# Optimization experiments

Hardware: AMD Instinct MI355X
Metric: run time of the kernel (lower is better)

The kernel has to match this reference:

```python
import jax, jax.numpy as jnp
import numpy as np

B, S, D, H, FF = 4, 2048, 1024, 16, 4096
DT, TARGET, ITERS = 0.1, 0.0, 5


def _ln(x, w, b):
    mu = jnp.mean(x, axis=-1, keepdims=True)
    var = jnp.mean((x - mu) ** 2, axis=-1, keepdims=True)
    return (x - mu) * jax.lax.rsqrt(var + 1e-5) * w + b


def setup_inputs() -> dict:
    key = jax.random.key(0)
    ks = iter(jax.random.split(key, 16))
    w = lambda shape: jax.random.normal(next(ks), shape, dtype=jnp.float32) * 0.02
    return {
        "x": jax.random.normal(next(ks), (B, S, D), dtype=jnp.float32),
        "ln_attn_w": jnp.ones((D,), jnp.float32), "ln_attn_b": jnp.zeros((D,), jnp.float32),
        "attn_in_w": w((3 * D, D)), "attn_in_b": jnp.zeros((3 * D,), jnp.float32),
        "attn_out_w": w((D, D)), "attn_out_b": jnp.zeros((D,), jnp.float32),
        "ln1_w": jnp.ones((D,), jnp.float32), "ln1_b": jnp.zeros((D,), jnp.float32),
        "ln2_w": jnp.ones((D,), jnp.float32), "ln2_b": jnp.zeros((D,), jnp.float32),
        "inl_u_w": w((D, D)), "inl_u_b": jnp.zeros((D,), jnp.float32),
        "inl_a_w": w((D, D)), "inl_a_b": jnp.zeros((D,), jnp.float32),
        "inl_b_w": w((D, D)), "inl_b_b": jnp.zeros((D,), jnp.float32),
        "inl_g_w": w((D, D)), "inl_g_b": jnp.zeros((D,), jnp.float32),
        "ff1_w": w((FF, D)), "ff1_b": jnp.zeros((FF,), jnp.float32),
        "ff2_w": w((D, FF)), "ff2_b": jnp.zeros((D,), jnp.float32),
    }


def reference(x, ln_attn_w, ln_attn_b, attn_in_w, attn_in_b, attn_out_w, attn_out_b,
              ln1_w, ln1_b, ln2_w, ln2_b,
              inl_u_w, inl_u_b, inl_a_w, inl_a_b, inl_b_w, inl_b_b, inl_g_w, inl_g_b,
              ff1_w, ff1_b, ff2_w, ff2_b):
    dh = D // H
    scale = 1.0 / np.sqrt(dh).astype(np.float32)
    # --- causal multi-head attention (dropout = identity, eval mode) ---
    xn = _ln(x, ln_attn_w, ln_attn_b)
    qkv = xn @ attn_in_w.T + attn_in_b            # [B,S,3D]
    q, k, v = jnp.split(qkv, 3, axis=-1)
    hsplit = lambda t: t.reshape(B, S, H, dh).transpose(0, 2, 1, 3)  # [B,H,S,dh]
    q, k, v = hsplit(q), hsplit(k), hsplit(v)
    scores = jnp.einsum('bhqd,bhkd->bhqk', q, k) * scale
    causal = jnp.triu(jnp.ones((S, S), dtype=bool), 1)
    scores = jnp.where(causal, jnp.finfo(scores.dtype).min, scores)
    probs = jax.nn.softmax(scores, axis=-1)
    attn_out = jnp.einsum('bhqk,bhkd->bhqd', probs, v).transpose(0, 2, 1, 3).reshape(B, S, D)
    attn_out = attn_out @ attn_out_w.T + attn_out_b
    x = x + attn_out
    context = attn_out
    # --- INL integrator dynamics (controllers depend only on context) ---
    xs = _ln(x, ln1_w, ln1_b)
    vs = jnp.zeros_like(xs)
    u = context @ inl_u_w.T + inl_u_b
    alpha = jax.nn.sigmoid(context @ inl_a_w.T + inl_a_b)
    beta = jax.nn.softplus(context @ inl_b_w.T + inl_b_b)
    g = jax.nn.sigmoid(context @ inl_g_w.T + inl_g_b)
    for _ in range(ITERS):
        vs = vs + DT * (alpha * (TARGET - xs) - beta * vs + u)
        xs = xs + DT * g * vs
    x = x + xs
    # --- feed-forward (exact GELU as torch default) ---
    h = _ln(x, ln2_w, ln2_b)
    x = x + (jax.nn.gelu(h @ ff1_w.T + ff1_b, approximate=False) @ ff2_w.T + ff2_b)
    return x
```

## Files before the change

kernel.cpp:

```cpp
#include <hip/hip_runtime.h>
#include <cstdint>
#include <cmath>

typedef __attribute__((ext_vector_type(4))) float floatx4;
typedef __attribute__((ext_vector_type(8))) __bf16 bf16x8;
typedef __attribute__((ext_vector_type(4))) unsigned short ushort4v;

#define DEVI static __device__ __forceinline__

DEVI unsigned short f2b(float f) {
    unsigned x = __float_as_uint(f);
    return (unsigned short)((x + 0x7fffu + ((x >> 16) & 1u)) >> 16);
}
DEVI float b2f(unsigned short u) { return __uint_as_float(((unsigned)u) << 16); }

DEVI void load16(void* lds, const void* g) {
    __builtin_amdgcn_global_load_lds(
        (__attribute__((address_space(1))) void*)(const_cast<void*>(g)),
        (__attribute__((address_space(3))) void*)lds, 16, 0, 0);
}

__global__ __launch_bounds__(256) void cvt_kernel(const float* __restrict__ src,
                                                  unsigned short* __restrict__ dst, int n4) {
    int i = blockIdx.x * 256 + threadIdx.x;
    if (i >= n4) return;
    floatx4 v = ((const floatx4*)src)[i];
    ushort4v o;
    o[0] = f2b(v[0]); o[1] = f2b(v[1]); o[2] = f2b(v[2]); o[3] = f2b(v[3]);
    ((ushort4v*)dst)[i] = o;
}

__global__ __launch_bounds__(256) void catbias_kernel(const float* __restrict__ a,
                                                      const float* __restrict__ b,
                                                      const float* __restrict__ c,
                                                      const float* __restrict__ d,
                                                      float* __restrict__ o) {
    int i = blockIdx.x * 256 + threadIdx.x;
    int p = i >> 10, j = i & 1023;
    float v = (p == 0) ? a[j] : (p == 1) ? b[j] : (p == 2) ? c[j] : d[j];
    o[i] = v;
}

__global__ __launch_bounds__(256) void ln_kernel(const float* __restrict__ in,
                                                 const float* __restrict__ w,
                                                 const float* __restrict__ b,
                                                 unsigned short* __restrict__ obf,
                                                 float* __restrict__ of) {
    const int row = blockIdx.x, tid = threadIdx.x;
    const floatx4* pr = (const floatx4*)(in + (size_t)row * 1024);
    floatx4 v = pr[tid];
    float s  = v[0] + v[1] + v[2] + v[3];
    float ss = v[0]*v[0] + v[1]*v[1] + v[2]*v[2] + v[3]*v[3];
    #pragma unroll
    for (int o = 32; o >= 1; o >>= 1) { s += __shfl_xor(s, o); ss += __shfl_xor(ss, o); }
    __shared__ float red[8];
    int wv = tid >> 6, lane = tid & 63;
    if (lane == 0) { red[wv] = s; red[4 + wv] = ss; }
    __syncthreads();
    s  = red[0] + red[1] + red[2] + red[3];
    ss = red[4] + red[5] + red[6] + red[7];
    float mu  = s * (1.0f / 1024.0f);
    float var = ss * (1.0f / 1024.0f) - mu * mu;
    float rstd = rsqrtf(var + 1e-5f);
    floatx4 wv4 = ((const floatx4*)w)[tid];
    floatx4 bv4 = ((const floatx4*)b)[tid];
    floatx4 o;
    #pragma unroll
    for (int c = 0; c < 4; c++) o[c] = (v[c] - mu) * rstd * wv4[c] + bv4[c];
    if (obf) {
        ushort4v t;
        t[0] = f2b(o[0]); t[1] = f2b(o[1]); t[2] = f2b(o[2]); t[3] = f2b(o[3]);
        ((ushort4v*)(obf + (size_t)row * 1024))[tid] = t;
    }
    if (of) ((floatx4*)(of + (size_t)row * 1024))[tid] = o;
}

__global__ __launch_bounds__(256) void integrator_kernel(const float* __restrict__ xs0,
                                                         const unsigned short* __restrict__ uabg,
                                                         float* __restrict__ xio) {
    size_t i = (size_t)blockIdx.x * 256 + threadIdx.x;
    size_t tok = i >> 8;
    int grp = (int)(i & 255) * 4;
    const unsigned short* ubase = uabg + tok * 4096 + grp;
    ushort4v uu = *(const ushort4v*)(ubase);
    ushort4v aa = *(const ushort4v*)(ubase + 1024);
    ushort4v bb = *(const ushort4v*)(ubase + 2048);
    ushort4v gg = *(const ushort4v*)(ubase + 3072);
    floatx4 xsv = ((const floatx4*)xs0)[i];
    floatx4 x1  = ((const floatx4*)xio)[i];
    floatx4 res;
    #pragma unroll
    for (int c = 0; c < 4; c++) {
        float u = b2f(uu[c]), a = b2f(aa[c]), bt = b2f(bb[c]), g = b2f(gg[c]);
        float xs = xsv[c], vs = 0.f;
        #pragma unroll
        for (int t = 0; t < 5; t++) {
            vs += 0.1f * (-a * xs - bt * vs + u);
            xs += 0.1f * g * vs;
        }
        res[c] = x1[c] + xs;
    }
    ((floatx4*)xio)[i] = res;
}

template <int EPI>
__global__ __launch_bounds__(256, 3) void gemm_bt(const unsigned short* __restrict__ A,
                                                  const unsigned short* __restrict__ W,
                                                  const float* __restrict__ bias, int K,
                                                  unsigned short* __restrict__ ob0,
                                                  unsigned short* __restrict__ ob1,
                                                  unsigned short* __restrict__ ob2,
                                                  float* __restrict__ of0,
                                                  const float* __restrict__ xres) {
    __shared__ unsigned short sA[3][128 * 32];
    __shared__ unsigned short sB[3][128 * 32];
    const int tid = threadIdx.x;
    const int wave = tid >> 6, lane = tid & 63;
    const int ln = lane & 15, quad = lane >> 4;
    const size_t m0 = (size_t)blockIdx.y * 128;
    const int n0 = blockIdx.x * 128;
    const int wm = (wave >> 1) * 64, wn = (wave & 1) * 64;

    const floatx4 z4 = {0.f, 0.f, 0.f, 0.f};
    floatx4 acc[4][4];
    #pragma unroll
    for (int mt = 0; mt < 4; mt++)
        #pragma unroll
        for (int nt = 0; nt < 4; nt++) acc[mt][nt] = z4;

    const int r16 = lane >> 2;
    const int gsw = (((lane & 3) ^ (r16 & 3) ^ ((r16 >> 2) & 3))) * 8;
    const int arow = wave * 16 + r16;
    const unsigned short* gA = A + (m0 + (size_t)arow) * K + gsw;
    const unsigned short* gB = W + ((size_t)(n0 + arow)) * K + gsw;
    const size_t rs64 = (size_t)64 * K;
    const int so = wave * 512;
    const int swr = ((quad ^ (ln & 3) ^ ((ln >> 2) & 3))) * 8;

    const int T = K >> 5;

    load16(&sA[0][so], gA);
    load16(&sA[0][so + 2048], gA + rs64);
    load16(&sB[0][so], gB);
    load16(&sB[0][so + 2048], gB + rs64);
    load16(&sA[1][so], gA + 32);
    load16(&sA[1][so + 2048], gA + rs64 + 32);
    load16(&sB[1][so], gB + 32);
    load16(&sB[1][so + 2048], gB + rs64 + 32);
    asm volatile("s_waitcnt vmcnt(4)" ::: "memory");
    asm volatile("s_barrier" ::: "memory");

    bf16x8 fa0[4], fb0[4], fa1[4], fb1[4];
    #pragma unroll
    for (int mt = 0; mt < 4; mt++)
        fa0[mt] = *(const bf16x8*)&sA[0][(wm + mt * 16 + ln) * 32 + swr];
    #pragma unroll
    for (int nt = 0; nt < 4; nt++)
        fb0[nt] = *(const bf16x8*)&sB[0][(wn + nt * 16 + ln) * 32 + swr];

    auto step = [&](int t, bf16x8* afc, bf16x8* bfc, bf16x8* afn, bf16x8* bfn) {
        if (t + 2 < T) {
            const int k = (t + 2) * 32;
            const int nb = (t + 2) % 3;
            load16(&sA[nb][so], gA + k);
            load16(&sA[nb][so + 2048], gA + rs64 + k);
            load16(&sB[nb][so], gB + k);
            load16(&sB[nb][so + 2048], gB + rs64 + k);
        }
        __builtin_amdgcn_sched_barrier(0);
        __builtin_amdgcn_s_setprio(1);
        #pragma unroll
        for (int mt = 0; mt < 4; mt++)
            #pragma unroll
            for (int nt = 0; nt < 4; nt++)
                acc[mt][nt] = __builtin_amdgcn_mfma_f32_16x16x32_bf16(afc[mt], bfc[nt], acc[mt][nt], 0, 0, 0);
        __builtin_amdgcn_s_setprio(0);
        __builtin_amdgcn_sched_barrier(0);
        if (t + 1 < T) {
            if (t + 2 < T) {
                asm volatile("s_waitcnt vmcnt(4) lgkmcnt(0)" ::: "memory");
            } else {
                asm volatile("s_waitcnt vmcnt(0) lgkmcnt(0)" ::: "memory");
            }
            asm volatile("s_barrier" ::: "memory");
            const int nb = (t + 1) % 3;
            afn[0] = *(const bf16x8*)&sA[nb][(wm + ln) * 32 + swr];
            #pragma unroll
            for (int nt = 0; nt < 4; nt++)
                bfn[nt] = *(const bf16x8*)&sB[nb][(wn + nt * 16 + ln) * 32 + swr];
            #pragma unroll
            for (int mt = 1; mt < 4; mt++)
                afn[mt] = *(const bf16x8*)&sA[nb][(wm + mt * 16 + ln) * 32 + swr];
        }
    };

    #pragma unroll 1
    for (int t = 0; t < T; t += 2) {
        step(t, fa0, fb0, fa1, fb1);
        step(t + 1, fa1, fb1, fa0, fb0);
    }

    const size_t rowb = m0 + wm + quad * 4;
    const int colb = n0 + wn + ln;
    #pragma unroll
    for (int mt = 0; mt < 4; mt++) {
        #pragma unroll
        for (int nt = 0; nt < 4; nt++) {
            const int n = colb + nt * 16;
            const float bs = bias[n];
            #pragma unroll
            for (int r = 0; r < 4; r++) {
                const size_t row = rowb + mt * 16 + r;
                float c = acc[mt][nt][r] + bs;
                if constexpr (EPI == 0) {
                    int sect = n >> 10, d1 = n & 1023, h = d1 >> 6, d = d1 & 63;
                    int bb = (int)(row >> 11), s = (int)(row & 2047);
                    size_t bh = (size_t)(bb * 16 + h);
                    if (sect == 0)      ob0[(bh * 2048 + s) * 64 + d] = f2b(c);
                    else if (sect == 1) ob1[(bh * 2048 + s) * 64 + d] = f2b(c);
                    else                ob2[(bh * 64 + d) * 2048 + s] = f2b(c);
                } else if constexpr (EPI == 1) {
                    size_t idx = row * 1024 + n;
                    ob0[idx] = f2b(c);
                    of0[idx] = xres[idx] + c;
                } else if constexpr (EPI == 2) {
                    int p = n >> 10;
                    float v;
                    if (p == 0)       v = c;
                    else if (p == 2)  v = fmaxf(c, 0.f) + log1pf(__expf(-fabsf(c)));
                    else              v = 1.f / (1.f + __expf(-c));
                    ob0[row * 4096 + n] = f2b(v);
                } else if constexpr (EPI == 3) {
                    float v = 0.5f * c * (1.f + erff(c * 0.70710678118654752f));
                    ob0[row * 4096 + n] = f2b(v);
                } else {
                    size_t idx = row * 1024 + n;
                    of0[idx] += c;
                }
            }
        }
    }
}

#define PSTR 72
__global__ __launch_bounds__(256, 3) void attn_kernel(const unsigned short* __restrict__ Qb,
                                                      const unsigned short* __restrict__ Kb,
                                                      const unsigned short* __restrict__ Vtb,
                                                      unsigned short* __restrict__ Ob) {
    __shared__ unsigned short sK[2][64 * 64];
    __shared__ unsigned short sVt[2][64 * 64];
    __shared__ unsigned short sQP[128 * PSTR];
    const int pr = blockIdx.x;
    const int bh = blockIdx.y;
    const int tid = threadIdx.x, wave = tid >> 6, lane = tid & 63;
    const int ln = lane & 15, quad = lane >> 4;
    const unsigned short* Q  = Qb  + (size_t)bh * 2048 * 64;
    const unsigned short* Kp = Kb  + (size_t)bh * 2048 * 64;
    const unsigned short* Vt = Vtb + (size_t)bh * 64 * 2048;

    const int rl  = lane >> 3;
    const int gsw = (((lane & 7) ^ rl)) * 8;
    const int sseg = wave * 2;
    const unsigned short* kbase = Kp + (size_t)(sseg * 8 + rl) * 64 + gsw;
    const unsigned short* vbase = Vt + (size_t)(sseg * 8 + rl) * 2048 + gsw;
    unsigned short* sP = &sQP[wave * 32 * PSTR];
    const int bb = bh >> 4, h = bh & 15;
    const floatx4 z4 = {0.f, 0.f, 0.f, 0.f};

    #pragma unroll 1
    for (int phase = 0; phase < 2; phase++) {
        const int qt = phase ? pr : (15 - pr);
        const int q0 = qt * 128;
        const int T = 2 * qt + 2;

        #pragma unroll
        for (int i = 0; i < 4; i++) {
            int s = wave * 4 + i;
            load16(&sQP[s * 512], Q + (size_t)(q0 + s * 8 + rl) * 64 + gsw);
        }
        load16(&sK[0][sseg * 512], kbase);
        load16(&sK[0][(sseg + 1) * 512], kbase + (size_t)8 * 64);
        load16(&sVt[0][sseg * 512], vbase);
        load16(&sVt[0][(sseg + 1) * 512], vbase + (size_t)8 * 2048);
        asm volatile("s_waitcnt vmcnt(0)" ::: "memory");
        asm volatile("s_barrier" ::: "memory");

        bf16x8 aq[2][2];
        #pragma unroll
        for (int mt = 0; mt < 2; mt++)
            #pragma unroll
            for (int ks = 0; ks < 2; ks++)
                aq[mt][ks] = *(const bf16x8*)&sQP[(wave * 32 + mt * 16 + ln) * 64 +
                                                  (((ks * 4 + quad) ^ (ln & 7)) * 8)];
        asm volatile("s_waitcnt lgkmcnt(0)" ::: "memory");
        asm volatile("s_barrier" ::: "memory");

        floatx4 Oacc[2][4];
        float m_run[2][4], l_run[2][4];
        #pragma unroll
        for (int mt = 0; mt < 2; mt++)
            #pragma unroll
            for (int j = 0; j < 4; j++) { Oacc[mt][j] = z4; m_run[mt][j] = -1e30f; l_run[mt][j] = 0.f; }

        const int wave_first = q0 + wave * 32;
        const int wave_last  = wave_first + 31;

        #pragma unroll 1
        for (int t = 0; t < T; t++) {
            const int kk0 = t * 64;
            const int cur = t & 1;
            if (t + 1 < T) {
                const unsigned short* kg = kbase + (size_t)(kk0 + 64) * 64;
                const unsigned short* vg = vbase + (size_t)(kk0 + 64);
                load16(&sK[cur ^ 1][sseg * 512], kg);
                load16(&sK[cur ^ 1][(sseg + 1) * 512], kg + (size_t)8 * 64);
                load16(&sVt[cur ^ 1][sseg * 512], vg);
                load16(&sVt[cur ^ 1][(sseg + 1) * 512], vg + (size_t)8 * 2048);
                asm volatile("s_waitcnt vmcnt(4)" ::: "memory");
            } else {
                asm volatile("s_waitcnt vmcnt(0)" ::: "memory");
            }
            asm volatile("s_barrier" ::: "memory");

            if (kk0 <= wave_last) {
                floatx4 Sc[2][4];
                #pragma unroll
                for (int mt = 0; mt < 2; mt++)
                    #pragma unroll
                    for (int nt = 0; nt < 4; nt++) Sc[mt][nt] = z4;
                __builtin_amdgcn_s_setprio(1);
                #pragma unroll
                for (int ks = 0; ks < 2; ks++) {
                    #pragma unroll
                    for (int nt = 0; nt < 4; nt++) {
                        bf16x8 bk = *(const bf16x8*)&sK[cur][(nt * 16 + ln) * 64 +
                                                             (((ks * 4 + quad) ^ (ln & 7)) * 8)];
                        #pragma unroll
                        for (int mt = 0; mt < 2; mt++)
                            Sc[mt][nt] = __builtin_amdgcn_mfma_f32_16x16x32_bf16(aq[mt][ks], bk, Sc[mt][nt], 0, 0, 0);
                    }
                }
                __builtin_amdgcn_s_setprio(0);
                const bool diag = (kk0 + 63 > wave_first);
                #pragma unroll
                for (int mt = 0; mt < 2; mt++)
                    #pragma unroll
                    for (int nt = 0; nt < 4; nt++)
                        #pragma unroll
                        for (int r = 0; r < 4; r++) {
                            float v = Sc[mt][nt][r] * 0.125f;
                            if (diag) {
                                int rowg = wave_first + mt * 16 + quad * 4 + r;
                                int colg = kk0 + nt * 16 + ln;
                                if (colg > rowg) v = -1e30f;
                            }
                            Sc[mt][nt][r] = v;
                        }
                float alpha[2][4];
                #pragma unroll
                for (int mt = 0; mt < 2; mt++)
                    #pragma unroll
                    for (int r = 0; r < 4; r++) {
                        float mx = fmaxf(fmaxf(Sc[mt][0][r], Sc[mt][1][r]), fmaxf(Sc[mt][2][r], Sc[mt][3][r]));
                        #pragma unroll
                        for (int off = 1; off < 16; off <<= 1) mx = fmaxf(mx, __shfl_xor(mx, off));
                        float mnew = fmaxf(m_run[mt][r], mx);
                        alpha[mt][r] = __expf(m_run[mt][r] - mnew);
                        m_run[mt][r] = mnew;
                    }
                #pragma unroll
                for (int mt = 0; mt < 2; mt++)
                    #pragma unroll
                    for (int r = 0; r < 4; r++) {
                        float rs = 0.f;
                        #pragma unroll
                        for (int nt = 0; nt < 4; nt++) {
                            float p = __expf(Sc[mt][nt][r] - m_run[mt][r]);
                            Sc[mt][nt][r] = p;
                            rs += p;
                        }
                        #pragma unroll
                        for (int off = 1; off < 16; off <<= 1) rs += __shfl_xor(rs, off);
                        l_run[mt][r] = l_run[mt][r] * alpha[mt][r] + rs;
                    }
                #pragma unroll
                for (int mt = 0; mt < 2; mt++)
                    #pragma unroll
                    for (int nt = 0; nt < 4; nt++)
                        #pragma unroll
                        for (int r = 0; r < 4; r++) Oacc[mt][nt][r] *= alpha[mt][r];
                #pragma unroll
                for (int mt = 0; mt < 2; mt++)
                    #pragma unroll
                    for (int nt = 0; nt < 4; nt++)
                        #pragma unroll
                        for (int r = 0; r < 4; r++)
                            sP[(mt * 16 + quad * 4 + r) * PSTR + nt * 16 + ln] = f2b(Sc[mt][nt][r]);
                __builtin_amdgcn_s_setprio(1);
                #pragma unroll
                for (int kp = 0; kp < 2; kp++) {
                    bf16x8 ap[2];
                    #pragma unroll
                    for (int mt = 0; mt < 2; mt++)
                        ap[mt] = *(const bf16x8*)&sP[(mt * 16 + ln) * PSTR + kp * 32 + quad * 8];
                    #pragma unroll
                    for (int nt = 0; nt < 4; nt++) {
                        bf16x8 bv = *(const bf16x8*)&sVt[cur][(nt * 16 + ln) * 64 +
                                                              (((kp * 4 + quad) ^ (ln & 7)) * 8)];
                        #pragma unroll
                        for (int mt = 0; mt < 2; mt++)
                            Oacc[mt][nt] = __builtin_amdgcn_mfma_f32_16x16x32_bf16(ap[mt], bv, Oacc[mt][nt], 0, 0, 0);
                    }
                }
                __builtin_amdgcn_s_setprio(0);
            }
            asm volatile("s_barrier" ::: "memory");
        }

        #pragma unroll
        for (int mt = 0; mt < 2; mt++)
            #pragma unroll
            for (int nt = 0; nt < 4; nt++)
                #pragma unroll
                for (int r = 0; r < 4; r++) {
                    float o = Oacc[mt][nt][r] / l_run[mt][r];
                    int srow = q0 + wave * 32 + mt * 16 + quad * 4 + r;
                    size_t tok = (size_t)bb * 2048 + srow;
                    Ob[tok * 1024 + h * 64 + nt * 16 + ln] = f2b(o);
                }
    }
}

extern "C" void kernel_launch(void* const* d_in, const int* in_sizes, int n_in,
                              void* d_out, int out_size, void* d_ws, size_t ws_size,
                              hipStream_t stream) {
    const float* x          = (const float*)d_in[0];
    const float* ln_attn_w  = (const float*)d_in[1];
    const float* ln_attn_b  = (const float*)d_in[2];
    const float* attn_in_w  = (const float*)d_in[3];
    const float* attn_in_b  = (const float*)d_in[4];
    const float* attn_out_w = (const float*)d_in[5];
    const float* attn_out_b = (const float*)d_in[6];
    const float* ln1_w      = (const float*)d_in[7];
    const float* ln1_b      = (const float*)d_in[8];
    const float* ln2_w      = (const float*)d_in[9];
    const float* ln2_b      = (const float*)d_in[10];
    const float* inl_u_w    = (const float*)d_in[11];
    const float* inl_u_b    = (const float*)d_in[12];
    const float* inl_a_w    = (const float*)d_in[13];
    const float* inl_a_b    = (const float*)d_in[14];
    const float* inl_b_w    = (const float*)d_in[15];
    const float* inl_b_b    = (const float*)d_in[16];
    const float* inl_g_w    = (const float*)d_in[17];
    const float* inl_g_b    = (const float*)d_in[18];
    const float* ff1_w      = (const float*)d_in[19];
    const float* ff1_b      = (const float*)d_in[20];
    const float* ff2_w      = (const float*)d_in[21];
    const float* ff2_b      = (const float*)d_in[22];
    float* out = (float*)d_out;

    char* ws = (char*)d_ws;
    unsigned short* Wqkv  = (unsigned short*)(ws);
    unsigned short* Wout  = (unsigned short*)(ws + 6291456);
    unsigned short* Winl  = (unsigned short*)(ws + 8388608);
    unsigned short* Wff1  = (unsigned short*)(ws + 16777216);
    unsigned short* Wff2  = (unsigned short*)(ws + 25165824);
    unsigned short* xnb   = (unsigned short*)(ws + 33554432);
    unsigned short* qb    = (unsigned short*)(ws + 50331648);
    unsigned short* kb    = (unsigned short*)(ws + 67108864);
    unsigned short* vtb   = (unsigned short*)(ws + 83886080);
    unsigned short* attnb = (unsigned short*)(ws + 100663296);
    unsigned short* ctxb  = (unsigned short*)(ws + 117440512);
    float*          xs    = (float*)(ws + 134217728);
    float*          bias4 = (float*)(ws + 167772160);
    unsigned short* uabg  = (unsigned short*)(ws + 50331648);
    unsigned short* ff1b  = (unsigned short*)(ws + 50331648);

    cvt_kernel<<<3072, 256, 0, stream>>>(attn_in_w, Wqkv, 786432);
    cvt_kernel<<<1024, 256, 0, stream>>>(attn_out_w, Wout, 262144);
    cvt_kernel<<<1024, 256, 0, stream>>>(inl_u_w, Winl + 0, 262144);
    cvt_kernel<<<1024, 256, 0, stream>>>(inl_a_w, Winl + 1048576, 262144);
    cvt_kernel<<<1024, 256, 0, stream>>>(inl_b_w, Winl + 2097152, 262144);
    cvt_kernel<<<1024, 256, 0, stream>>>(inl_g_w, Winl + 3145728, 262144);
    cvt_kernel<<<4096, 256, 0, stream>>>(ff1_w, Wff1, 1048576);
    cvt_kernel<<<4096, 256, 0, stream>>>(ff2_w, Wff2, 1048576);
    catbias_kernel<<<16, 256, 0, stream>>>(inl_u_b, inl_a_b, inl_b_b, inl_g_b, bias4);

    ln_kernel<<<8192, 256, 0, stream>>>(x, ln_attn_w, ln_attn_b, xnb, nullptr);
    gemm_bt<0><<<dim3(24, 64), 256, 0, stream>>>(xnb, Wqkv, attn_in_b, 1024, qb, kb, vtb, nullptr, nullptr);
    attn_kernel<<<dim3(8, 64), 256, 0, stream>>>(qb, kb, vtb, attnb);
    gemm_bt<1><<<dim3(8, 64), 256, 0, stream>>>(attnb, Wout, attn_out_b, 1024, ctxb, nullptr, nullptr, out, x);
    ln_kernel<<<8192, 256, 0, stream>>>(out, ln1_w, ln1_b, nullptr, xs);
    gemm_bt<2><<<dim3(32, 64), 256, 0, stream>>>(ctxb, Winl, bias4, 1024, uabg, nullptr, nullptr, nullptr, nullptr);
    integrator_kernel<<<8192, 256, 0, stream>>>(xs, uabg, out);
    ln_kernel<<<8192, 256, 0, stream>>>(out, ln2_w, ln2_b, xnb, nullptr);
    gemm_bt<3><<<dim3(32, 64), 256, 0, stream>>>(xnb, Wff1, ff1_b, 1024, ff1b, nullptr, nullptr, nullptr, nullptr);
    gemm_bt<4><<<dim3(8, 64), 256, 0, stream>>>(ff1b, Wff2, ff2_b, 4096, nullptr, nullptr, nullptr, out, nullptr);
}
```

Measured before the change: 865.4 us.

## Add 256x256-tile 8-wave GEMM for wide projections and swizzle block order

Adds a new gemm8 kernel with 256x256 output tiles, 512 threads (8 waves, each 128x64), double-buffered LDS staging of 64-wide K slices, and an XCD-aware block remapping. It is used for the QKV, INL controller and FF1 GEMMs. The existing 128x128 kernel also gets the same block-index remap. The larger tiles increase operand reuse per LDS load, at the cost of more barriers per step and fewer blocks per grid (384-512), which may hurt occupancy and tail balance.

After: 912.5 us. 5.5% more time.

```diff
diff --git a/kernel.cpp b/kernel.cpp
--- a/kernel.cpp
+++ b/kernel.cpp
@@ -18,6 +18,10 @@
     __builtin_amdgcn_global_load_lds(
         (__attribute__((address_space(1))) void*)(const_cast<void*>(g)),
         (__attribute__((address_space(3))) void*)lds, 16, 0, 0);
+}
+
+DEVI floatx4 MFMA16(bf16x8 a, bf16x8 b, floatx4 c) {
+    return __builtin_amdgcn_mfma_f32_16x16x32_bf16(a, b, c, 0, 0, 0);
 }
 
 __global__ __launch_bounds__(256) void cvt_kernel(const float* __restrict__ src,
@@ -103,6 +107,162 @@
     ((floatx4*)xio)[i] = res;
 }
 
+template <int EPI, int KP>
+__global__ __launch_bounds__(512, 2) void gemm8(const unsigned short* __restrict__ A,
+                                                const unsigned short* __restrict__ W,
+                                                const float* __restrict__ bias,
+                                                unsigned short* __restrict__ ob0,
+                                                unsigned short* __restrict__ ob1,
+                                                unsigned short* __restrict__ ob2,
+                                                float* __restrict__ of0,
+                                                const float* __restrict__ xres) {
+    constexpr int NT = KP / 64;
+    __shared__ unsigned short sA[2][2][256 * 32];
+    __shared__ unsigned short sB[2][2][256 * 32];
+    const int tid = threadIdx.x;
+    const int wave = tid >> 6, lane = tid & 63;
+    const int ln = lane & 15, quad = lane >> 4;
+    const int wr = wave >> 2, wc = wave & 3;
+
+    const int gx = gridDim.x;
+    const int flat = blockIdx.y * gx + blockIdx.x;
+    const int cpx = (gx * (int)gridDim.y) >> 3;
+    const int rmp = (flat & 7) * cpx + (flat >> 3);
+    const size_t m0 = (size_t)(rmp / gx) * 256;
+    const int n0 = (rmp % gx) * 256;
+
+    floatx4 acc[8][4];
+    #pragma unroll
+    for (int mt = 0; mt < 8; mt++)
+        #pragma unroll
+        for (int nt = 0; nt < 4; nt++) acc[mt][nt] = floatx4{0.f, 0.f, 0.f, 0.f};
+
+    const int srow = tid >> 2;
+    const int sgr  = (tid & 3) ^ (srow & 3);
+    const unsigned short* gAs = A + (m0 + srow) * KP + sgr * 8;
+    const unsigned short* gBs = W + ((size_t)(n0 + srow)) * KP + sgr * 8;
+    const size_t jstride = (size_t)128 * KP;
+    const int sbase = wave * 512;
+
+    const int csw  = (quad ^ (ln & 3)) * 8;
+    const int arow = (wr * 128 + ln) * 32 + csw;
+    const int brow = (wc * 64 + ln) * 32 + csw;
+
+    auto stageA = [&](int buf, int kk, int t) {
+        const unsigned short* s = gAs + (size_t)t * 64 + kk * 32;
+        load16(&sA[buf][kk][sbase], s);
+        load16(&sA[buf][kk][sbase + 4096], s + jstride);
+    };
+    auto stageB = [&](int buf, int kk, int t) {
+        const unsigned short* s = gBs + (size_t)t * 64 + kk * 32;
+        load16(&sB[buf][kk][sbase], s);
+        load16(&sB[buf][kk][sbase + 4096], s + jstride);
+    };
+
+    bf16x8 af[8], bq0, bq1;
+    auto ldA = [&](int buf, int kk) {
+        #pragma unroll
+        for (int mt = 0; mt < 8; mt++)
+            af[mt] = *(const bf16x8*)&sA[buf][kk][arow + mt * 512];
+    };
+    auto ldB = [&](int buf, int kk, int nh) {
+        bq0 = *(const bf16x8*)&sB[buf][kk][brow + nh * 1024];
+        bq1 = *(const bf16x8*)&sB[buf][kk][brow + nh * 1024 + 512];
+    };
+    auto mma = [&](int nh) {
+        __builtin_amdgcn_sched_barrier(0);
+        __builtin_amdgcn_s_setprio(1);
+        #pragma unroll
+        for (int mt = 0; mt < 8; mt++) {
+            acc[mt][nh * 2]     = MFMA16(af[mt], bq0, acc[mt][nh * 2]);
+            acc[mt][nh * 2 + 1] = MFMA16(af[mt], bq1, acc[mt][nh * 2 + 1]);
+        }
+        __builtin_amdgcn_s_setprio(0);
+        __builtin_amdgcn_sched_barrier(0);
+    };
+
+    stageA(0, 0, 0); stageB(0, 0, 0); stageA(0, 1, 0); stageB(0, 1, 0);
+    asm volatile("s_waitcnt vmcnt(4)" ::: "memory");
+    asm volatile("s_barrier" ::: "memory");
+
+    auto tilestep = [&](int kt, int buf, bool last) {
+        ldA(buf, 0); ldB(buf, 0, 0);
+        if (!last) stageA(buf ^ 1, 0, kt + 1);
+        asm volatile("s_barrier" ::: "memory");
+        asm volatile("s_waitcnt lgkmcnt(0)" ::: "memory");
+        mma(0);
+        asm volatile("s_barrier" ::: "memory");
+        ldB(buf, 0, 1);
+        if (!last) {
+            stageB(buf ^ 1, 0, kt + 1);
+            asm volatile("s_waitcnt vmcnt(4)" ::: "memory");
+        } else {
+            asm volatile("s_waitcnt vmcnt(0)" ::: "memory");
+        }
+        asm volatile("s_barrier" ::: "memory");
+        asm volatile("s_waitcnt lgkmcnt(0)" ::: "memory");
+        mma(1);
+        asm volatile("s_barrier" ::: "memory");
+        ldA(buf, 1); ldB(buf, 1, 0);
+        if (!last) stageA(buf ^ 1, 1, kt + 1);
+        asm volatile("s_barrier" ::: "memory");
+        asm volatile("s_waitcnt lgkmcnt(0)" ::: "memory");
+        mma(0);
+        asm volatile("s_barrier" ::: "memory");
+        ldB(buf, 1, 1);
+        if (!last) {
+            stageB(buf ^ 1, 1, kt + 1);
+            asm volatile("s_waitcnt vmcnt(4)" ::: "memory");
+        }
+        asm volatile("s_barrier" ::: "memory");
+        asm volatile("s_waitcnt lgkmcnt(0)" ::: "memory");
+        mma(1);
+        asm volatile("s_barrier" ::: "memory");
+    };
+
+    #pragma unroll 1
+    for (int kt = 0; kt < NT - 2; kt += 2) {
+        tilestep(kt, 0, false);
+        tilestep(kt + 1, 1, false);
+    }
+    tilestep(NT - 2, 0, false);
+    tilestep(NT - 1, 1, true);
+
+    const size_t rowb = m0 + wr * 128 + quad * 4;
+    const int colb = n0 + wc * 64 + ln;
+    #pragma unroll
+    for (int mt = 0; mt < 8; mt++) {
+        #pragma unroll
+        for (int nt = 0; nt < 4; nt++) {
+            const int n = colb + nt * 16;
+            const float bs = bias[n];
+            #pragma unroll
+            for (int r = 0; r < 4; r++) {
+                const size_t row = rowb + mt * 16 + r;
+                float c = acc[mt][nt][r] + bs;
+                if constexpr (EPI == 0) {
+                    int sect = n >> 10, d1 = n & 1023, h = d1 >> 6, d = d1 & 63;
+                    int bb = (int)(row >> 11), s = (int)(row & 2047);
+                    size_t bh = (size_t)(bb * 16 + h);
+                    if (sect == 0)      ob0[(bh * 2048 + s) * 64 + d] = f2b(c);
+                    else if (sect == 1) ob1[(bh * 2048 + s) * 64 + d] = f2b(c);
+                    else                ob2[(bh * 64 + d) * 2048 + s] = f2b(c);
+                } else if constexpr (EPI == 2) {
+                    int p = n >> 10;
+                    float v;
+                    if (p == 0)       v = c;
+                    else if (p == 2)  v = fmaxf(c, 0.f) + log1pf(__expf(-fabsf(c)));
+                    else              v = 1.f / (1.f + __expf(-c));
+                    ob0[row * 4096 + n] = f2b(v);
+                } else if constexpr (EPI == 3) {
+                    float v = 0.5f * c * (1.f + erff(c * 0.70710678118654752f));
+                    ob0[row * 4096 + n] = f2b(v);
+                }
+            }
+        }
+    }
+}
+
 template <int EPI>
 __global__ __launch_bounds__(256, 3) void gemm_bt(const unsigned short* __restrict__ A,
                                                   const unsigned short* __restrict__ W,
@@ -117,8 +277,12 @@
     const int tid = threadIdx.x;
     const int wave = tid >> 6, lane = tid & 63;
     const int ln = lane & 15, quad = lane >> 4;
-    const size_t m0 = (size_t)blockIdx.y * 128;
-    const int n0 = blockIdx.x * 128;
+    const int gx = gridDim.x;
+    const int flat = blockIdx.y * gx + blockIdx.x;
+    const int cpx = (gx * (int)gridDim.y) >> 3;
+    const int rmp = (flat & 7) * cpx + (flat >> 3);
+    const size_t m0 = (size_t)(rmp / gx) * 128;
+    const int n0 = (rmp % gx) * 128;
     const int wm = (wave >> 1) * 64, wn = (wave & 1) * 64;
 
     const floatx4 z4 = {0.f, 0.f, 0.f, 0.f};
@@ -173,7 +337,7 @@
         for (int mt = 0; mt < 4; mt++)
             #pragma unroll
             for (int nt = 0; nt < 4; nt++)
-                acc[mt][nt] = __builtin_amdgcn_mfma_f32_16x16x32_bf16(afc[mt], bfc[nt], acc[mt][nt], 0, 0, 0);
+                acc[mt][nt] = MFMA16(afc[mt], bfc[nt], acc[mt][nt]);
         __builtin_amdgcn_s_setprio(0);
         __builtin_amdgcn_sched_barrier(0);
         if (t + 1 < T) {
@@ -212,27 +376,10 @@
             for (int r = 0; r < 4; r++) {
                 const size_t row = rowb + mt * 16 + r;
                 float c = acc[mt][nt][r] + bs;
-                if constexpr (EPI == 0) {
-                    int sect = n >> 10, d1 = n & 1023, h = d1 >> 6, d = d1 & 63;
-                    int bb = (int)(row >> 11), s = (int)(row & 2047);
-                    size_t bh = (size_t)(bb * 16 + h);
-                    if (sect == 0)      ob0[(bh * 2048 + s) * 64 + d] = f2b(c);
-                    else if (sect == 1) ob1[(bh * 2048 + s) * 64 + d] = f2b(c);
-                    else                ob2[(bh * 64 + d) * 2048 + s] = f2b(c);
-                } else if constexpr (EPI == 1) {
+                if constexpr (EPI == 1) {
                     size_t idx = row * 1024 + n;
                     ob0[idx] = f2b(c);
                     of0[idx] = xres[idx] + c;
-                } else if constexpr (EPI == 2) {
-                    int p = n >> 10;
-                    float v;
-                    if (p == 0)       v = c;
-                    else if (p == 2)  v = fmaxf(c, 0.f) + log1pf(__expf(-fabsf(c)));
-                    else              v = 1.f / (1.f + __expf(-c));
-                    ob0[row * 4096 + n] = f2b(v);
-                } else if constexpr (EPI == 3) {
-                    float v = 0.5f * c * (1.f + erff(c * 0.70710678118654752f));
-                    ob0[row * 4096 + n] = f2b(v);
                 } else {
                     size_t idx = row * 1024 + n;
                     of0[idx] += c;
@@ -337,7 +484,7 @@
                                                              (((ks * 4 + quad) ^ (ln & 7)) * 8)];
                         #pragma unroll
                         for (int mt = 0; mt < 2; mt++)
-                            Sc[mt][nt] = __builtin_amdgcn_mfma_f32_16x16x32_bf16(aq[mt][ks], bk, Sc[mt][nt], 0, 0, 0);
+                            Sc[mt][nt] = MFMA16(aq[mt][ks], bk, Sc[mt][nt]);
                     }
                 }
                 __builtin_amdgcn_s_setprio(0);
@@ -409,7 +556,7 @@
                                                               (((kp * 4 + quad) ^ (ln & 7)) * 8)];
                         #pragma unroll
                         for (int mt = 0; mt < 2; mt++)
-                            Oacc[mt][nt] = __builtin_amdgcn_mfma_f32_16x16x32_bf16(ap[mt], bv, Oacc[mt][nt], 0, 0, 0);
+                            Oacc[mt][nt] = MFMA16(ap[mt], bv, Oacc[mt][nt]);
                     }
                 }
                 __builtin_amdgcn_s_setprio(0);
@@ -487,13 +634,13 @@
     catbias_kernel<<<16, 256, 0, stream>>>(inl_u_b, inl_a_b, inl_b_b, inl_g_b, bias4);
 
     ln_kernel<<<8192, 256, 0, stream>>>(x, ln_attn_w, ln_attn_b, xnb, nullptr);
-    gemm_bt<0><<<dim3(24, 64), 256, 0, stream>>>(xnb, Wqkv, attn_in_b, 1024, qb, kb, vtb, nullptr, nullptr);
+    gemm8<0, 1024><<<dim3(12, 32), 512, 0, stream>>>(xnb, Wqkv, attn_in_b, qb, kb, vtb, nullptr, nullptr);
     attn_kernel<<<dim3(8, 64), 256, 0, stream>>>(qb, kb, vtb, attnb);
     gemm_bt<1><<<dim3(8, 64), 256, 0, stream>>>(attnb, Wout, attn_out_b, 1024, ctxb, nullptr, nullptr, out, x);
     ln_kernel<<<8192, 256, 0, stream>>>(out, ln1_w, ln1_b, nullptr, xs);
-    gemm_bt<2><<<dim3(32, 64), 256, 0, stream>>>(ctxb, Winl, bias4, 1024, uabg, nullptr, nullptr, nullptr, nullptr);
+    gemm8<2, 1024><<<dim3(16, 32), 512, 0, stream>>>(ctxb, Winl, bias4, uabg, nullptr, nullptr, nullptr, nullptr);
     integrator_kernel<<<8192, 256, 0, stream>>>(xs, uabg, out);
     ln_kernel<<<8192, 256, 0, stream>>>(out, ln2_w, ln2_b, xnb, nullptr);
-    gemm_bt<3><<<dim3(32, 64), 256, 0, stream>>>(xnb, Wff1, ff1_b, 1024, ff1b, nullptr, nullptr, nullptr, nullptr);
+    gemm8<3, 1024><<<dim3(16, 32), 512, 0, stream>>>(xnb, Wff1, ff1_b, ff1b, nullptr, nullptr, nullptr, nullptr);
     gemm_bt<4><<<dim3(8, 64), 256, 0, stream>>>(ff1b, Wff2, ff2_b, 4096, nullptr, nullptr, nullptr, out, nullptr);
 }
```

## Simplify GEMM to double-buffered LDS, raise occupancy, add XCD-aware block remap

Applied to the files above, without the earlier changes.

Replaces the GEMM's three-stage LDS ring and register-prefetched fragments with a simple two-stage double buffer that loads fragments right before the MFMAs. This cuts LDS and register use so launch bounds can ask for four blocks per SIMD instead of three. It also remaps block indices so that consecutive tiles are spread across the 8 XCD chiplets, which should improve L2 locality. The cost is less latency hiding: each step waits for all global loads and for the LDS reads before its MFMAs start.

New measurement: 901.0 us. 1.04x slower.

```diff
diff --git a/kernel.cpp b/kernel.cpp
--- a/kernel.cpp
+++ b/kernel.cpp
@@ -18,6 +18,10 @@
     __builtin_amdgcn_global_load_lds(
         (__attribute__((address_space(1))) void*)(const_cast<void*>(g)),
         (__attribute__((address_space(3))) void*)lds, 16, 0, 0);
+}
+
+DEVI floatx4 MFMA16(bf16x8 a, bf16x8 b, floatx4 c) {
+    return __builtin_amdgcn_mfma_f32_16x16x32_bf16(a, b, c, 0, 0, 0);
 }
 
 __global__ __launch_bounds__(256) void cvt_kernel(const float* __restrict__ src,
@@ -104,7 +108,7 @@
 }
 
 template <int EPI>
-__global__ __launch_bounds__(256, 3) void gemm_bt(const unsigned short* __restrict__ A,
+__global__ __launch_bounds__(256, 4) void gemm_bt(const unsigned short* __restrict__ A,
                                                   const unsigned short* __restrict__ W,
                                                   const float* __restrict__ bias, int K,
                                                   unsigned short* __restrict__ ob0,
@@ -112,13 +116,17 @@
                                                   unsigned short* __restrict__ ob2,
                                                   float* __restrict__ of0,
                                                   const float* __restrict__ xres) {
-    __shared__ unsigned short sA[3][128 * 32];
-    __shared__ unsigned short sB[3][128 * 32];
+    __shared__ unsigned short sA[2][128 * 32];
+    __shared__ unsigned short sB[2][128 * 32];
     const int tid = threadIdx.x;
     const int wave = tid >> 6, lane = tid & 63;
     const int ln = lane & 15, quad = lane >> 4;
-    const size_t m0 = (size_t)blockIdx.y * 128;
-    const int n0 = blockIdx.x * 128;
+    const int gx = gridDim.x;
+    const int flat = blockIdx.y * gx + blockIdx.x;
+    const int cpx = (gx * (int)gridDim.y) >> 3;
+    const int rmp = (flat & 7) * cpx + (flat >> 3);
+    const size_t m0 = (size_t)(rmp / gx) * 128;
+    const int n0 = (rmp % gx) * 128;
     const int wm = (wave >> 1) * 64, wn = (wave & 1) * 64;
 
     const floatx4 z4 = {0.f, 0.f, 0.f, 0.f};
@@ -143,61 +151,41 @@
     load16(&sA[0][so + 2048], gA + rs64);
     load16(&sB[0][so], gB);
     load16(&sB[0][so + 2048], gB + rs64);
-    load16(&sA[1][so], gA + 32);
-    load16(&sA[1][so + 2048], gA + rs64 + 32);
-    load16(&sB[1][so], gB + 32);
-    load16(&sB[1][so + 2048], gB + rs64 + 32);
-    asm volatile("s_waitcnt vmcnt(4)" ::: "memory");
+    asm volatile("s_waitcnt vmcnt(0)" ::: "memory");
     asm volatile("s_barrier" ::: "memory");
 
-    bf16x8 fa0[4], fb0[4], fa1[4], fb1[4];
-    #pragma unroll
-    for (int mt = 0; mt < 4; mt++)
-        fa0[mt] = *(const bf16x8*)&sA[0][(wm + mt * 16 + ln) * 32 + swr];
-    #pragma unroll
-    for (int nt = 0; nt < 4; nt++)
-        fb0[nt] = *(const bf16x8*)&sB[0][(wn + nt * 16 + ln) * 32 + swr];
-
-    auto step = [&](int t, bf16x8* afc, bf16x8* bfc, bf16x8* afn, bf16x8* bfn) {
-        if (t + 2 < T) {
-            const int k = (t + 2) * 32;
-            const int nb = (t + 2) % 3;
-            load16(&sA[nb][so], gA + k);
-            load16(&sA[nb][so + 2048], gA + rs64 + k);
-            load16(&sB[nb][so], gB + k);
-            load16(&sB[nb][so + 2048], gB + rs64 + k);
-        }
+    #pragma unroll 1
+    for (int t = 0; t < T; t++) {
+        const int c = t & 1;
+        if (t + 1 < T) {
+            const int k = (t + 1) * 32;
+            load16(&sA[c ^ 1][so], gA + k);
+            load16(&sA[c ^ 1][so + 2048], gA + rs64 + k);
+            load16(&sB[c ^ 1][so], gB + k);
+            load16(&sB[c ^ 1][so + 2048], gB + rs64 + k);
+        }
+        __builtin_amdgcn_sched_barrier(0);
+        bf16x8 fa[4], fb[4];
+        #pragma unroll
+        for (int mt = 0; mt < 4; mt++)
+            fa[mt] = *(const bf16x8*)&sA[c][(wm + mt * 16 + ln) * 32 + swr];
+        #pragma unroll
+        for (int nt = 0; nt < 4; nt++)
+            fb[nt] = *(const bf16x8*)&sB[c][(wn + nt * 16 + ln) * 32 + swr];
+        asm volatile("s_waitcnt lgkmcnt(0)" ::: "memory");
         __builtin_amdgcn_sched_barrier(0);
         __builtin_amdgcn_s_setprio(1);
         #pragma unroll
         for (int mt = 0; mt < 4; mt++)
             #pragma unroll
             for (int nt = 0; nt < 4; nt++)
-                acc[mt][nt] = __builtin_amdgcn_mfma_f32_16x16x32_bf16(afc[mt], bfc[nt], acc[mt][nt], 0, 0, 0);
+                acc[mt][nt] = MFMA16(fa[mt], fb[nt], acc[mt][nt]);
         __builtin_amdgcn_s_setprio(0);
         __builtin_amdgcn_sched_barrier(0);
         if (t + 1 < T) {
-            if (t + 2 < T) {
-                asm volatile("s_waitcnt vmcnt(4) lgkmcnt(0)" ::: "memory");
-            } else {
-                asm volatile("s_waitcnt vmcnt(0) lgkmcnt(0)" ::: "memory");
-            }
+            asm volatile("s_waitcnt vmcnt(0)" ::: "memory");
             asm volatile("s_barrier" ::: "memory");
-            const int nb = (t + 1) % 3;
-            afn[0] = *(const bf16x8*)&sA[nb][(wm + ln) * 32 + swr];
-            #pragma unroll
-            for (int nt = 0; nt < 4; nt++)
-                bfn[nt] = *(const bf16x8*)&sB[nb][(wn + nt * 16 + ln) * 32 + swr];
-            #pragma unroll
-            for (int mt = 1; mt < 4; mt++)
-                afn[mt] = *(const bf16x8*)&sA[nb][(wm + mt * 16 + ln) * 32 + swr];
-        }
-    };
-
-    #pragma unroll 1
-    for (int t = 0; t < T; t += 2) {
-        step(t, fa0, fb0, fa1, fb1);
-        step(t + 1, fa1, fb1, fa0, fb0);
+        }
     }
 
     const size_t rowb = m0 + wm + quad * 4;
@@ -337,7 +325,7 @@
                                                              (((ks * 4 + quad) ^ (ln & 7)) * 8)];
                         #pragma unroll
                         for (int mt = 0; mt < 2; mt++)
-                            Sc[mt][nt] = __builtin_amdgcn_mfma_f32_16x16x32_bf16(aq[mt][ks], bk, Sc[mt][nt], 0, 0, 0);
+                            Sc[mt][nt] = MFMA16(aq[mt][ks], bk, Sc[mt][nt]);
                     }
                 }
                 __builtin_amdgcn_s_setprio(0);
@@ -409,7 +397,7 @@
                                                               (((kp * 4 + quad) ^ (ln & 7)) * 8)];
                         #pragma unroll
                         for (int mt = 0; mt < 2; mt++)
-                            Oacc[mt][nt] = __builtin_amdgcn_mfma_f32_16x16x32_bf16(ap[mt], bv, Oacc[mt][nt], 0, 0, 0);
+                            Oacc[mt][nt] = MFMA16(ap[mt], bv, Oacc[mt][nt]);
                     }
                 }
                 __builtin_amdgcn_s_setprio(0);
```

## Fuse LN1, integrator and LN2 into one kernel; merge weight conversions

Applied to the files above, without the earlier changes.

Replaces the separate LN1 kernel, the integrator kernel and the LN2 kernel with a single per-row kernel. It computes LN1 inline, runs the integrator, writes the residual and then computes LN2 to bf16. This removes the fp32 xs intermediate and several full-tensor global reads and writes. The eight weight-conversion launches are also merged into one launch, and an MFMA wrapper is added for readability. The fused kernel uses two block-wide reductions per row.

Result: no change. 860.2 us (-0.6%).

```diff
diff --git a/kernel.cpp b/kernel.cpp
--- a/kernel.cpp
+++ b/kernel.cpp
@@ -20,14 +20,38 @@
         (__attribute__((address_space(3))) void*)lds, 16, 0, 0);
 }
 
-__global__ __launch_bounds__(256) void cvt_kernel(const float* __restrict__ src,
-                                                  unsigned short* __restrict__ dst, int n4) {
+DEVI floatx4 MFMA16(bf16x8 a, bf16x8 b, floatx4 c) {
+    return __builtin_amdgcn_mfma_f32_16x16x32_bf16(a, b, c, 0, 0, 0);
+}
+
+__global__ __launch_bounds__(256) void cvt_all(const float* __restrict__ s0,
+                                               const float* __restrict__ s1,
+                                               const float* __restrict__ s2,
+                                               const float* __restrict__ s3,
+                                               const float* __restrict__ s4,
+                                               const float* __restrict__ s5,
+                                               const float* __restrict__ s6,
+                                               const float* __restrict__ s7,
+                                               unsigned short* d0, unsigned short* d1,
+                                               unsigned short* d2, unsigned short* d3,
+                                               unsigned short* d4, unsigned short* d5,
+                                               unsigned short* d6, unsigned short* d7) {
     int i = blockIdx.x * 256 + threadIdx.x;
-    if (i >= n4) return;
-    floatx4 v = ((const floatx4*)src)[i];
+    int seg = i >> 18;
+    int j = i & 262143;
+    const float* src; unsigned short* dst;
+    if (seg < 3)        { src = s0; dst = d0; j += seg * 262144; }
+    else if (seg == 3)  { src = s1; dst = d1; }
+    else if (seg == 4)  { src = s2; dst = d2; }
+    else if (seg == 5)  { src = s3; dst = d3; }
+    else if (seg == 6)  { src = s4; dst = d4; }
+    else if (seg == 7)  { src = s5; dst = d5; }
+    else if (seg < 12)  { src = s6; dst = d6; j += (seg - 8) * 262144; }
+    else                { src = s7; dst = d7; j += (seg - 12) * 262144; }
+    floatx4 v = ((const floatx4*)src)[j];
     ushort4v o;
     o[0] = f2b(v[0]); o[1] = f2b(v[1]); o[2] = f2b(v[2]); o[3] = f2b(v[3]);
-    ((ushort4v*)dst)[i] = o;
+    ((ushort4v*)dst)[j] = o;
 }
 
 __global__ __launch_bounds__(256) void catbias_kernel(const float* __restrict__ a,
@@ -44,8 +68,7 @@
 __global__ __launch_bounds__(256) void ln_kernel(const float* __restrict__ in,
                                                  const float* __restrict__ w,
                                                  const float* __restrict__ b,
-                                                 unsigned short* __restrict__ obf,
-                                                 float* __restrict__ of) {
+                                                 unsigned short* __restrict__ obf) {
     const int row = blockIdx.x, tid = threadIdx.x;
     const floatx4* pr = (const floatx4*)(in + (size_t)row * 1024);
     floatx4 v = pr[tid];
@@ -64,43 +87,73 @@
     float rstd = rsqrtf(var + 1e-5f);
     floatx4 wv4 = ((const floatx4*)w)[tid];
     floatx4 bv4 = ((const floatx4*)b)[tid];
-    floatx4 o;
-    #pragma unroll
-    for (int c = 0; c < 4; c++) o[c] = (v[c] - mu) * rstd * wv4[c] + bv4[c];
-    if (obf) {
-        ushort4v t;
-        t[0] = f2b(o[0]); t[1] = f2b(o[1]); t[2] = f2b(o[2]); t[3] = f2b(o[3]);
-        ((ushort4v*)(obf + (size_t)row * 1024))[tid] = t;
-    }
-    if (of) ((floatx4*)(of + (size_t)row * 1024))[tid] = o;
-}
-
-__global__ __launch_bounds__(256) void integrator_kernel(const float* __restrict__ xs0,
-                                                         const unsigned short* __restrict__ uabg,
-                                                         float* __restrict__ xio) {
-    size_t i = (size_t)blockIdx.x * 256 + threadIdx.x;
-    size_t tok = i >> 8;
-    int grp = (int)(i & 255) * 4;
-    const unsigned short* ubase = uabg + tok * 4096 + grp;
+    ushort4v t;
+    #pragma unroll
+    for (int c = 0; c < 4; c++) t[c] = f2b((v[c] - mu) * rstd * wv4[c] + bv4[c]);
+    ((ushort4v*)(obf + (size_t)row * 1024))[tid] = t;
+}
+
+__global__ __launch_bounds__(256) void integrator_ln_kernel(const float* __restrict__ w1,
+                                                            const float* __restrict__ b1,
+                                                            const float* __restrict__ w2,
+                                                            const float* __restrict__ b2,
+                                                            const unsigned short* __restrict__ uabg,
+                                                            float* __restrict__ xio,
+                                                            unsigned short* __restrict__ hb) {
+    const int row = blockIdx.x, tid = threadIdx.x;
+    const int wv = tid >> 6, lane = tid & 63;
+    __shared__ float red[8], red2[8];
+
+    floatx4 v = ((const floatx4*)(xio + (size_t)row * 1024))[tid];
+    float s  = v[0] + v[1] + v[2] + v[3];
+    float ss = v[0]*v[0] + v[1]*v[1] + v[2]*v[2] + v[3]*v[3];
+    #pragma unroll
+    for (int o = 32; o >= 1; o >>= 1) { s += __shfl_xor(s, o); ss += __shfl_xor(ss, o); }
+    if (lane == 0) { red[wv] = s; red[4 + wv] = ss; }
+    __syncthreads();
+    s  = red[0] + red[1] + red[2] + red[3];
+    ss = red[4] + red[5] + red[6] + red[7];
+    float mu  = s * (1.0f / 1024.0f);
+    float rstd = rsqrtf(ss * (1.0f / 1024.0f) - mu * mu + 1e-5f);
+    floatx4 w1v = ((const floatx4*)w1)[tid];
+    floatx4 b1v = ((const floatx4*)b1)[tid];
+
+    const unsigned short* ubase = uabg + (size_t)row * 4096 + tid * 4;
     ushort4v uu = *(const ushort4v*)(ubase);
     ushort4v aa = *(const ushort4v*)(ubase + 1024);
     ushort4v bb = *(const ushort4v*)(ubase + 2048);
     ushort4v gg = *(const ushort4v*)(ubase + 3072);
-    floatx4 xsv = ((const floatx4*)xs0)[i];
-    floatx4 x1  = ((const floatx4*)xio)[i];
     floatx4 res;
     #pragma unroll
     for (int c = 0; c < 4; c++) {
+        float xs = (v[c] - mu) * rstd * w1v[c] + b1v[c];
         float u = b2f(uu[c]), a = b2f(aa[c]), bt = b2f(bb[c]), g = b2f(gg[c]);
-        float xs = xsv[c], vs = 0.f;
+        float vs = 0.f;
         #pragma unroll
         for (int t = 0; t < 5; t++) {
             vs += 0.1f * (-a * xs - bt * vs + u);
             xs += 0.1f * g * vs;
         }
-        res[c] = x1[c] + xs;
+        res[c] = v[c] + xs;
     }
-    ((floatx4*)xio)[i] = res;
+    ((floatx4*)(xio + (size_t)row * 1024))[tid] = res;
+
+    float s2  = res[0] + res[1] + res[2] + res[3];
+    float ss2 = res[0]*res[0] + res[1]*res[1] + res[2]*res[2] + res[3]*res[3];
+    #pragma unroll
+    for (int o = 32; o >= 1; o >>= 1) { s2 += __shfl_xor(s2, o); ss2 += __shfl_xor(ss2, o); }
+    if (lane == 0) { red2[wv] = s2; red2[4 + wv] = ss2; }
+    __syncthreads();
+    s2  = red2[0] + red2[1] + red2[2] + red2[3];
+    ss2 = red2[4] + red2[5] + red2[6] + red2[7];
+    float mu2  = s2 * (1.0f / 1024.0f);
+    float rstd2 = rsqrtf(ss2 * (1.0f / 1024.0f) - mu2 * mu2 + 1e-5f);
+    floatx4 w2v = ((const floatx4*)w2)[tid];
+    floatx4 b2v = ((const floatx4*)b2)[tid];
+    ushort4v t;
+    #pragma unroll
+    for (int c = 0; c < 4; c++) t[c] = f2b((res[c] - mu2) * rstd2 * w2v[c] + b2v[c]);
+    ((ushort4v*)(hb + (size_t)row * 1024))[tid] = t;
 }
 
 template <int EPI>
@@ -173,7 +226,7 @@
         for (int mt = 0; mt < 4; mt++)
             #pragma unroll
             for (int nt = 0; nt < 4; nt++)
-                acc[mt][nt] = __builtin_amdgcn_mfma_f32_16x16x32_bf16(afc[mt], bfc[nt], acc[mt][nt], 0, 0, 0);
+                acc[mt][nt] = MFMA16(afc[mt], bfc[nt], acc[mt][nt]);
         __builtin_amdgcn_s_setprio(0);
         __builtin_amdgcn_sched_barrier(0);
         if (t + 1 < T) {
@@ -337,7 +390,7 @@
                                                              (((ks * 4 + quad) ^ (ln & 7)) * 8)];
                         #pragma unroll
                         for (int mt = 0; mt < 2; mt++)
-                            Sc[mt][nt] = __builtin_amdgcn_mfma_f32_16x16x32_bf16(aq[mt][ks], bk, Sc[mt][nt], 0, 0, 0);
+                            Sc[mt][nt] = MFMA16(aq[mt][ks], bk, Sc[mt][nt]);
                     }
                 }
                 __builtin_amdgcn_s_setprio(0);
@@ -409,7 +462,7 @@
                                                               (((kp * 4 + quad) ^ (ln & 7)) * 8)];
                         #pragma unroll
                         for (int mt = 0; mt < 2; mt++)
-                            Oacc[mt][nt] = __builtin_amdgcn_mfma_f32_16x16x32_bf16(ap[mt], bv, Oacc[mt][nt], 0, 0, 0);
+                            Oacc[mt][nt] = MFMA16(ap[mt], bv, Oacc[mt][nt]);
                     }
                 }
                 __builtin_amdgcn_s_setprio(0);
@@ -471,29 +524,22 @@
     unsigned short* vtb   = (unsigned short*)(ws + 83886080);
     unsigned short* attnb = (unsigned short*)(ws + 100663296);
     unsigned short* ctxb  = (unsigned short*)(ws + 117440512);
-    float*          xs    = (float*)(ws + 134217728);
     float*          bias4 = (float*)(ws + 167772160);
     unsigned short* uabg  = (unsigned short*)(ws + 50331648);
     unsigned short* ff1b  = (unsigned short*)(ws + 50331648);
 
-    cvt_kernel<<<3072, 256, 0, stream>>>(attn_in_w, Wqkv, 786432);
-    cvt_kernel<<<1024, 256, 0, stream>>>(attn_out_w, Wout, 262144);
-    cvt_kernel<<<1024, 256, 0, stream>>>(inl_u_w, Winl + 0, 262144);
-    cvt_kernel<<<1024, 256, 0, stream>>>(inl_a_w, Winl + 1048576, 262144);
-    cvt_kernel<<<1024, 256, 0, stream>>>(inl_b_w, Winl + 2097152, 262144);
-    cvt_kernel<<<1024, 256, 0, stream>>>(inl_g_w, Winl + 3145728, 262144);
-    cvt_kernel<<<4096, 256, 0, stream>>>(ff1_w, Wff1, 1048576);
-    cvt_kernel<<<4096, 256, 0, stream>>>(ff2_w, Wff2, 1048576);
+    cvt_all<<<16384, 256, 0, stream>>>(attn_in_w, attn_out_w, inl_u_w, inl_a_w,
+                                       inl_b_w, inl_g_w, ff1_w, ff2_w,
+                                       Wqkv, Wout, Winl, Winl + 1048576,
+                                       Winl + 2097152, Winl + 3145728, Wff1, Wff2);
     catbias_kernel<<<16, 256, 0, stream>>>(inl_u_b, inl_a_b, inl_b_b, inl_g_b, bias4);
 
-    ln_kernel<<<8192, 256, 0, stream>>>(x, ln_attn_w, ln_attn_b, xnb, nullptr);
+    ln_kernel<<<8192, 256, 0, stream>>>(x, ln_attn_w, ln_attn_b, xnb);
     gemm_bt<0><<<dim3(24, 64), 256, 0, stream>>>(xnb, Wqkv, attn_in_b, 1024, qb, kb, vtb, nullptr, nullptr);
     attn_kernel<<<dim3(8, 64), 256, 0, stream>>>(qb, kb, vtb, attnb);
     gemm_bt<1><<<dim3(8, 64), 256, 0, stream>>>(attnb, Wout, attn_out_b, 1024, ctxb, nullptr, nullptr, out, x);
-    ln_kernel<<<8192, 256, 0, stream>>>(out, ln1_w, ln1_b, nullptr, xs);
     gemm_bt<2><<<dim3(32, 64), 256, 0, stream>>>(ctxb, Winl, bias4, 1024, uabg, nullptr, nullptr, nullptr, nullptr);
-    integrator_kernel<<<8192, 256, 0, stream>>>(xs, uabg, out);
-    ln_kernel<<<8192, 256, 0, stream>>>(out, ln2_w, ln2_b, xnb, nullptr);
+    integrator_ln_kernel<<<8192, 256, 0, stream>>>(ln1_w, ln1_b, ln2_w, ln2_b, uabg, out, xnb);
     gemm_bt<3><<<dim3(32, 64), 256, 0, stream>>>(xnb, Wff1, ff1_b, 1024, ff1b, nullptr, nullptr, nullptr, nullptr);
     gemm_bt<4><<<dim3(8, 64), 256, 0, stream>>>(ff1b, Wff2, ff2_b, 4096, nullptr, nullptr, nullptr, out, nullptr);
 }
```
